# Optimization experiments

Hardware: AMD Instinct MI355X
Metric: run time of the kernel (lower is better)

Reference implementation:

```python
import jax, jax.numpy as jnp
import numpy as np

N_NODES = 50000
N_EDGES = 400000
D = 256
EDGE_DIM = 64
N_LAYERS = 3


def setup_inputs() -> dict:
    key = jax.random.key(0)
    ks = jax.random.split(key, 8)
    sc = 1.0 / np.sqrt(D)
    x = jax.random.normal(ks[0], (N_NODES, D), dtype=jnp.float32)
    edge_attr = jax.random.normal(ks[1], (N_EDGES, EDGE_DIM), dtype=jnp.float32)
    edge_index = jax.random.randint(ks[2], (2, N_EDGES), 0, N_NODES, dtype=jnp.int64)
    Wl = jax.random.normal(ks[3], (N_LAYERS, D, D), dtype=jnp.float32) * sc
    bl = jax.random.normal(ks[4], (N_LAYERS, D), dtype=jnp.float32) * 0.01
    Wr = jax.random.normal(ks[5], (N_LAYERS, D, D), dtype=jnp.float32) * sc
    We = jax.random.normal(ks[6], (N_LAYERS, D, EDGE_DIM), dtype=jnp.float32) * (1.0 / np.sqrt(EDGE_DIM))
    be = jax.random.normal(ks[7], (N_LAYERS, D), dtype=jnp.float32) * 0.01
    return {"x": x, "edge_attr": edge_attr, "edge_index": edge_index,
            "Wl": Wl, "bl": bl, "Wr": Wr, "We": We, "be": be}


def reference(x, edge_attr, edge_index, Wl, bl, Wr, We, be):
    # SAGEConv (mean aggr, root_weight=True, no normalize) with edge-feature
    # augmented messages: msg = x[src] + edge_lin(edge_attr)
    src, dst = edge_index[0], edge_index[1]
    n = x.shape[0]
    # per-target in-degree for mean aggregation (computed once; edge_index fixed)
    deg = jax.ops.segment_sum(jnp.ones((edge_index.shape[1],), x.dtype), dst,
                              num_segments=n)
    inv_deg = (1.0 / jnp.maximum(deg, 1.0))[:, None]  # [N,1]
    for l in range(Wl.shape[0]):
        e_msg = edge_attr @ We[l].T + be[l]                 # [E,D] edge_lin
        msg = x[src] + e_msg                                 # gather + add
        agg = jax.ops.segment_sum(msg, dst, num_segments=n) * inv_deg  # mean
        x = jax.nn.relu(agg @ Wl[l].T + bl[l] + x @ Wr[l].T)
    return x
```

## Files before the change

kernel.cpp:

```cpp
#include <hip/hip_runtime.h>

typedef __attribute__((ext_vector_type(8))) short bf16x8;
typedef __attribute__((ext_vector_type(4))) float f32x4;
typedef unsigned short u16;

#define AS1 __attribute__((address_space(1)))
#define AS3 __attribute__((address_space(3)))

__device__ __forceinline__ u16 f2bf(float f) {
    union { float f; unsigned u; } v; v.f = f;
    unsigned u = v.u;
    return (u16)((u + 0x7FFFu + ((u >> 16) & 1u)) >> 16);
}
__device__ __forceinline__ float bf2f(u16 h) {
    union { unsigned u; float f; } v; v.u = ((unsigned)h) << 16;
    return v.f;
}

__global__ __launch_bounds__(256) void k_convert(const float* __restrict__ x,
                                                 u16* __restrict__ hb, int total4) {
    int i = blockIdx.x * 256 + threadIdx.x;
    if (i >= total4) return;
    float4 v = ((const float4*)x)[i];
    ushort4 o;
    o.x = f2bf(v.x); o.y = f2bf(v.y); o.z = f2bf(v.z); o.w = f2bf(v.w);
    ((ushort4*)hb)[i] = o;
}

__global__ __launch_bounds__(256) void k_count(const int* __restrict__ dst,
                                               int* __restrict__ deg, int E) {
    int e = blockIdx.x * 256 + threadIdx.x;
    if (e < E) atomicAdd(&deg[dst[e]], 1);
}

__global__ __launch_bounds__(256) void k_part(const int* __restrict__ deg,
                                              int* __restrict__ part, int N) {
    __shared__ int ws[4];
    int i = blockIdx.x * 256 + threadIdx.x;
    int v = (i < N) ? deg[i] : 0;
#pragma unroll
    for (int o = 32; o; o >>= 1) v += __shfl_down(v, o);
    int lane = threadIdx.x & 63, w = threadIdx.x >> 6;
    if (lane == 0) ws[w] = v;
    __syncthreads();
    if (threadIdx.x == 0) part[blockIdx.x] = ws[0] + ws[1] + ws[2] + ws[3];
}

__global__ __launch_bounds__(256) void k_scanp(const int* __restrict__ part,
                                               int* __restrict__ bases, int P) {
    __shared__ int s[256];
    int t = threadIdx.x;
    int v = (t < P) ? part[t] : 0;
    s[t] = v;
    __syncthreads();
#pragma unroll
    for (int o = 1; o < 256; o <<= 1) {
        int u = (t >= o) ? s[t - o] : 0;
        __syncthreads();
        s[t] += u;
        __syncthreads();
    }
    bases[t] = s[t] - v;
}

__global__ __launch_bounds__(256) void k_apply(const int* __restrict__ deg,
                                               const int* __restrict__ bases,
                                               int* __restrict__ rp, int* __restrict__ cur,
                                               int N, int E) {
    __shared__ int s[256];
    int b = blockIdx.x, t = threadIdx.x;
    int i = b * 256 + t;
    int d = (i < N) ? deg[i] : 0;
    s[t] = d;
    __syncthreads();
#pragma unroll
    for (int o = 1; o < 256; o <<= 1) {
        int u = (t >= o) ? s[t - o] : 0;
        __syncthreads();
        s[t] += u;
        __syncthreads();
    }
    if (i < N) {
        int r = bases[b] + s[t] - d;
        rp[i] = r;
        cur[i] = r;
    }
    if (b == (int)gridDim.x - 1 && t == 255) rp[N] = E;
}

__global__ __launch_bounds__(256) void k_fill(const int* __restrict__ dst, const int* __restrict__ src,
                                              int* __restrict__ cur,
                                              int* __restrict__ eid, int* __restrict__ srcs, int E) {
    int e = blockIdx.x * 256 + threadIdx.x;
    if (e < E) {
        int p = atomicAdd(&cur[dst[e]], 1);
        eid[p] = e;
        srcs[p] = src[e];
    }
}

__global__ __launch_bounds__(256) void k_sa(const float* __restrict__ attr, const int* __restrict__ rp,
                                            const int* __restrict__ eid, u16* __restrict__ Sa,
                                            unsigned char* __restrict__ hasdeg, int N) {
    int v = blockIdx.x * 4 + (threadIdx.x >> 6);
    if (v >= N) return;
    int l = threadIdx.x & 63;
    int g = l >> 4;
    int c = (l & 15) * 4;
    int j0 = rp[v], j1 = rp[v + 1];
    float4 a = {0.f, 0.f, 0.f, 0.f};
    int jc = j1 - 1;
    for (int j = j0; j < j1; j += 8) {
        int i0 = j + g;
        int i1 = j + 4 + g;
        float m0 = (i0 < j1) ? 1.f : 0.f;
        float m1 = (i1 < j1) ? 1.f : 0.f;
        int e0 = eid[i0 < jc ? i0 : jc];
        int e1 = eid[i1 < jc ? i1 : jc];
        float4 x0 = *(const float4*)&attr[(size_t)e0 * 64 + c];
        float4 x1 = *(const float4*)&attr[(size_t)e1 * 64 + c];
        a.x += m0 * x0.x + m1 * x1.x;
        a.y += m0 * x0.y + m1 * x1.y;
        a.z += m0 * x0.z + m1 * x1.z;
        a.w += m0 * x0.w + m1 * x1.w;
    }
    a.x += __shfl_xor(a.x, 16); a.y += __shfl_xor(a.y, 16);
    a.z += __shfl_xor(a.z, 16); a.w += __shfl_xor(a.w, 16);
    a.x += __shfl_xor(a.x, 32); a.y += __shfl_xor(a.y, 32);
    a.z += __shfl_xor(a.z, 32); a.w += __shfl_xor(a.w, 32);
    int dg = j1 - j0;
    float m = 1.f / (float)(dg > 1 ? dg : 1);
    if (l < 16) {
        ushort4 o;
        o.x = f2bf(a.x * m); o.y = f2bf(a.y * m);
        o.z = f2bf(a.z * m); o.w = f2bf(a.w * m);
        *(ushort4*)&Sa[(size_t)v * 64 + c] = o;
        if (l == 0) hasdeg[v] = (dg > 0) ? 1 : 0;
    }
}

__global__ __launch_bounds__(256) void k_sx(const u16* __restrict__ hb, const int* __restrict__ rp,
                                            const int* __restrict__ srcs,
                                            u16* __restrict__ Sx, int N) {
    int v = blockIdx.x * 4 + (threadIdx.x >> 6);
    if (v >= N) return;
    int l = threadIdx.x & 63;
    int h = l >> 5;
    int c = (l & 31) * 8;
    int j0 = rp[v], j1 = rp[v + 1];
    float a[8] = {0.f, 0.f, 0.f, 0.f, 0.f, 0.f, 0.f, 0.f};
    int jc = j1 - 1;
    for (int j = j0; j < j1; j += 8) {
        int i0 = j + h;
        int i1 = j + 2 + h;
        int i2 = j + 4 + h;
        int i3 = j + 6 + h;
        float m0 = (i0 < j1) ? 1.f : 0.f;
        float m1 = (i1 < j1) ? 1.f : 0.f;
        float m2 = (i2 < j1) ? 1.f : 0.f;
        float m3 = (i3 < j1) ? 1.f : 0.f;
        int s0 = srcs[i0 < jc ? i0 : jc];
        int s1 = srcs[i1 < jc ? i1 : jc];
        int s2 = srcs[i2 < jc ? i2 : jc];
        int s3 = srcs[i3 < jc ? i3 : jc];
        bf16x8 u0 = *(const bf16x8*)&hb[(size_t)s0 * 256 + c];
        bf16x8 u1 = *(const bf16x8*)&hb[(size_t)s1 * 256 + c];
        bf16x8 u2 = *(const bf16x8*)&hb[(size_t)s2 * 256 + c];
        bf16x8 u3 = *(const bf16x8*)&hb[(size_t)s3 * 256 + c];
#pragma unroll
        for (int i = 0; i < 8; ++i)
            a[i] += (m0 * bf2f((u16)u0[i]) + m1 * bf2f((u16)u1[i]))
                  + (m2 * bf2f((u16)u2[i]) + m3 * bf2f((u16)u3[i]));
    }
#pragma unroll
    for (int i = 0; i < 8; ++i) a[i] += __shfl_xor(a[i], 32);
    int dg = j1 - j0;
    float m = 1.f / (float)(dg > 1 ? dg : 1);
    if (l < 32) {
        bf16x8 o;
#pragma unroll
        for (int i = 0; i < 8; ++i) o[i] = (short)f2bf(a[i] * m);
        *(bf16x8*)&Sx[(size_t)v * 256 + c] = o;
    }
}

__global__ __launch_bounds__(256) void k_wprep(const float* __restrict__ Wl, const float* __restrict__ Wr,
                                               const float* __restrict__ We, const float* __restrict__ be,
                                               u16* __restrict__ Wlb, u16* __restrict__ Wrb,
                                               u16* __restrict__ Wleb, float* __restrict__ wlbe) {
    int t = blockIdx.x * 256 + threadIdx.x;
    if (t < 3 * 65536) { Wlb[t] = f2bf(Wl[t]); Wrb[t] = f2bf(Wr[t]); }
    if (t < 3 * 16384) {
        int l = t >> 14;
        int r = t & 16383;
        int d = r >> 6, jj = r & 63;
        const float* wl = Wl + ((size_t)l << 16) + (size_t)d * 256;
        const float* we = We + ((size_t)l << 14) + jj;
        float s = 0.f;
        for (int p = 0; p < 256; ++p) s += wl[p] * we[(size_t)p * 64];
        Wleb[t] = f2bf(s);
    }
    if (t < 768) {
        int l = t >> 8, d = t & 255;
        const float* wl = Wl + ((size_t)l << 16) + (size_t)d * 256;
        const float* b = be + l * 256;
        float s = 0.f;
        for (int p = 0; p < 256; ++p) s += wl[p] * b[p];
        wlbe[t] = s;
    }
}

__device__ __forceinline__ void do_seg(const u16* __restrict__ A, const u16* __restrict__ B,
                                       int lda, int K, int r0, int c0, int M,
                                       u16* Alds, u16* Blds,
                                       int lane, int w, int wr, int wc,
                                       int r16, int kq, f32x4 (&acc)[4][4]) {
    const int rloc = lane >> 3;
    const int cE = (lane & 7) * 8;
    for (int k0 = 0; k0 < K; k0 += 64) {
        __syncthreads();
#pragma unroll
        for (int i = 0; i < 4; ++i) {
            int ch = w * 4 + i;
            int ar = r0 + ch * 8 + rloc;
            ar = ar < M ? ar : M - 1;
            __builtin_amdgcn_global_load_lds(
                (const AS1 void*)(A + (size_t)ar * lda + k0 + cE),
                (AS3 void*)(Alds + ch * 512), 16, 0, 0);
            int br = c0 + ch * 8 + rloc;
            __builtin_amdgcn_global_load_lds(
                (const AS1 void*)(B + (size_t)br * K + k0 + cE),
                (AS3 void*)(Blds + ch * 512), 16, 0, 0);
        }
        __syncthreads();
        bf16x8 af[4][2], bfr[4][2];
#pragma unroll
        for (int rf = 0; rf < 4; ++rf) {
            af[rf][0] = *(const bf16x8*)&Alds[(wr * 64 + rf * 16 + r16) * 64 + kq];
            af[rf][1] = *(const bf16x8*)&Alds[(wr * 64 + rf * 16 + r16) * 64 + 32 + kq];
        }
#pragma unroll
        for (int cf = 0; cf < 4; ++cf) {
            bfr[cf][0] = *(const bf16x8*)&Blds[(wc * 64 + cf * 16 + r16) * 64 + kq];
            bfr[cf][1] = *(const bf16x8*)&Blds[(wc * 64 + cf * 16 + r16) * 64 + 32 + kq];
        }
#pragma unroll
        for (int rf = 0; rf < 4; ++rf)
#pragma unroll
            for (int cf = 0; cf < 4; ++cf) {
                acc[rf][cf] = __builtin_amdgcn_mfma_f32_16x16x32_bf16(af[rf][0], bfr[cf][0], acc[rf][cf], 0, 0, 0);
                acc[rf][cf] = __builtin_amdgcn_mfma_f32_16x16x32_bf16(af[rf][1], bfr[cf][1], acc[rf][cf], 0, 0, 0);
            }
    }
}

__global__ __launch_bounds__(256, 4) void k_gemm(
    const u16* __restrict__ Sx, const u16* __restrict__ Hb, const u16* __restrict__ Sa,
    const u16* __restrict__ Wlb, const u16* __restrict__ Wrb, const u16* __restrict__ Wleb,
    const float* __restrict__ bl, const float* __restrict__ wlbe,
    const unsigned char* __restrict__ hasdeg,
    u16* hb_out, float* f_out, int M)
{
    __shared__ __align__(16) u16 Alds[128 * 64];
    __shared__ __align__(16) u16 Blds[128 * 64];
    const int tid = threadIdx.x;
    const int lane = tid & 63;
    const int w = tid >> 6;
    const int wr = w & 1, wc = w >> 1;
    const int r16 = lane & 15;
    const int hi = lane >> 4;
    const int kq = hi * 8;
    const int rb = blockIdx.x >> 1;
    const int cb = blockIdx.x & 1;
    const int r0 = rb * 128;
    const int c0 = cb * 128;

    const f32x4 fzero = {0.f, 0.f, 0.f, 0.f};
    f32x4 acc[4][4];
#pragma unroll
    for (int a = 0; a < 4; ++a)
#pragma unroll
        for (int b = 0; b < 4; ++b) acc[a][b] = fzero;

    do_seg(Sx, Wlb, 256, 256, r0, c0, M, Alds, Blds, lane, w, wr, wc, r16, kq, acc);
    do_seg(Hb, Wrb, 256, 256, r0, c0, M, Alds, Blds, lane, w, wr, wc, r16, kq, acc);
    do_seg(Sa, Wleb, 64, 64, r0, c0, M, Alds, Blds, lane, w, wr, wc, r16, kq, acc);

    float blv[4], wbev[4];
#pragma unroll
    for (int cf = 0; cf < 4; ++cf) {
        int col = c0 + wc * 64 + 16 * cf + r16;
        blv[cf] = bl[col];
        wbev[cf] = wlbe[col];
    }
#pragma unroll
    for (int rf = 0; rf < 4; ++rf)
#pragma unroll
        for (int j = 0; j < 4; ++j) {
            int r = r0 + wr * 64 + 16 * rf + 4 * hi + j;
            if (r < M) {
                float hd = hasdeg[r] ? 1.f : 0.f;
#pragma unroll
                for (int cf = 0; cf < 4; ++cf) {
                    int col = c0 + wc * 64 + 16 * cf + r16;
                    float v = acc[rf][cf][j] + blv[cf] + hd * wbev[cf];
                    v = fmaxf(v, 0.f);
                    if (f_out) f_out[(size_t)r * 256 + col] = v;
                    if (hb_out) hb_out[(size_t)r * 256 + col] = f2bf(v);
                }
            }
        }
}

extern "C" void kernel_launch(void* const* d_in, const int* in_sizes, int n_in,
                              void* d_out, int out_size, void* d_ws, size_t ws_size,
                              hipStream_t stream) {
    const float* x    = (const float*)d_in[0];
    const float* attr = (const float*)d_in[1];
    const int*   ei   = (const int*)d_in[2];
    const float* Wl   = (const float*)d_in[3];
    const float* bl   = (const float*)d_in[4];
    const float* Wr   = (const float*)d_in[5];
    const float* We   = (const float*)d_in[6];
    const float* be   = (const float*)d_in[7];
    float* out = (float*)d_out;

    const int N = in_sizes[0] / 256;
    const int E = in_sizes[1] / 64;
    const int* srcA = ei;
    const int* dstA = ei + E;

    char* p = (char*)d_ws;
    auto carve = [&](size_t bytes) -> char* {
        char* q = p;
        p += (bytes + 255) & ~(size_t)255;
        return q;
    };
    u16* hb0    = (u16*)carve((size_t)N * 256 * 2);
    u16* hb1    = (u16*)carve((size_t)N * 256 * 2);
    u16* SxB    = (u16*)carve((size_t)N * 256 * 2);
    u16* SaB    = (u16*)carve((size_t)N * 64 * 2);
    u16* Wlb    = (u16*)carve((size_t)3 * 65536 * 2);
    u16* Wrb    = (u16*)carve((size_t)3 * 65536 * 2);
    u16* Wleb   = (u16*)carve((size_t)3 * 16384 * 2);
    float* wlbe = (float*)carve((size_t)3 * 256 * 4);
    int* deg    = (int*)carve((size_t)N * 4);
    int* rp     = (int*)carve((size_t)(N + 1) * 4);
    int* cur    = (int*)carve((size_t)N * 4);
    int* eid    = (int*)carve((size_t)E * 4);
    int* srcs   = (int*)carve((size_t)E * 4);
    int* part   = (int*)carve((size_t)256 * 4);
    int* bases  = (int*)carve((size_t)256 * 4);
    unsigned char* hasdeg = (unsigned char*)carve((size_t)N);

    hipMemsetAsync(deg, 0, (size_t)N * 4, stream);

    int t4 = N * 64;
    k_convert<<<(t4 + 255) / 256, 256, 0, stream>>>(x, hb0, t4);
    k_count<<<(E + 255) / 256, 256, 0, stream>>>(dstA, deg, E);
    const int PB = (N + 255) / 256;
    k_part<<<PB, 256, 0, stream>>>(deg, part, N);
    k_scanp<<<1, 256, 0, stream>>>(part, bases, PB);
    k_apply<<<PB, 256, 0, stream>>>(deg, bases, rp, cur, N, E);
    k_fill<<<(E + 255) / 256, 256, 0, stream>>>(dstA, srcA, cur, eid, srcs, E);
    k_sa<<<(N + 3) / 4, 256, 0, stream>>>(attr, rp, eid, SaB, hasdeg, N);
    k_wprep<<<(3 * 65536 + 255) / 256, 256, 0, stream>>>(Wl, Wr, We, be, Wlb, Wrb, Wleb, wlbe);

    const int RB = (N + 127) / 128;
    const int gblocks = RB * 2;
    u16* hcur = hb0;
    u16* hnxt = hb1;
    for (int l = 0; l < 3; ++l) {
        k_sx<<<(N + 3) / 4, 256, 0, stream>>>(hcur, rp, srcs, SxB, N);
        k_gemm<<<gblocks, 256, 0, stream>>>(SxB, hcur, SaB,
            Wlb + l * 65536, Wrb + l * 65536, Wleb + l * 16384,
            bl + l * 256, wlbe + l * 256, hasdeg,
            (l < 2) ? hnxt : (u16*)nullptr, (l == 2) ? out : (float*)nullptr, N);
        u16* t = hcur; hcur = hnxt; hnxt = t;
    }
}
```

Measured before the change: 319.7 us.

## Cover all 256 output columns per GEMM block with 512 threads

```diff
diff --git a/kernel.cpp b/kernel.cpp
--- a/kernel.cpp
+++ b/kernel.cpp
@@ -210,51 +210,7 @@
     }
 }
 
-__device__ __forceinline__ void do_seg(const u16* __restrict__ A, const u16* __restrict__ B,
-                                       int lda, int K, int r0, int c0, int M,
-                                       u16* Alds, u16* Blds,
-                                       int lane, int w, int wr, int wc,
-                                       int r16, int kq, f32x4 (&acc)[4][4]) {
-    const int rloc = lane >> 3;
-    const int cE = (lane & 7) * 8;
-    for (int k0 = 0; k0 < K; k0 += 64) {
-        __syncthreads();
-#pragma unroll
-        for (int i = 0; i < 4; ++i) {
-            int ch = w * 4 + i;
-            int ar = r0 + ch * 8 + rloc;
-            ar = ar < M ? ar : M - 1;
-            __builtin_amdgcn_global_load_lds(
-                (const AS1 void*)(A + (size_t)ar * lda + k0 + cE),
-                (AS3 void*)(Alds + ch * 512), 16, 0, 0);
-            int br = c0 + ch * 8 + rloc;
-            __builtin_amdgcn_global_load_lds(
-                (const AS1 void*)(B + (size_t)br * K + k0 + cE),
-                (AS3 void*)(Blds + ch * 512), 16, 0, 0);
-        }
-        __syncthreads();
-        bf16x8 af[4][2], bfr[4][2];
-#pragma unroll
-        for (int rf = 0; rf < 4; ++rf) {
-            af[rf][0] = *(const bf16x8*)&Alds[(wr * 64 + rf * 16 + r16) * 64 + kq];
-            af[rf][1] = *(const bf16x8*)&Alds[(wr * 64 + rf * 16 + r16) * 64 + 32 + kq];
-        }
-#pragma unroll
-        for (int cf = 0; cf < 4; ++cf) {
-            bfr[cf][0] = *(const bf16x8*)&Blds[(wc * 64 + cf * 16 + r16) * 64 + kq];
-            bfr[cf][1] = *(const bf16x8*)&Blds[(wc * 64 + cf * 16 + r16) * 64 + 32 + kq];
-        }
-#pragma unroll
-        for (int rf = 0; rf < 4; ++rf)
-#pragma unroll
-            for (int cf = 0; cf < 4; ++cf) {
-                acc[rf][cf] = __builtin_amdgcn_mfma_f32_16x16x32_bf16(af[rf][0], bfr[cf][0], acc[rf][cf], 0, 0, 0);
-                acc[rf][cf] = __builtin_amdgcn_mfma_f32_16x16x32_bf16(af[rf][1], bfr[cf][1], acc[rf][cf], 0, 0, 0);
-            }
-    }
-}
-
-__global__ __launch_bounds__(256, 4) void k_gemm(
+__global__ __launch_bounds__(512, 4) void k_gemm(
     const u16* __restrict__ Sx, const u16* __restrict__ Hb, const u16* __restrict__ Sa,
     const u16* __restrict__ Wlb, const u16* __restrict__ Wrb, const u16* __restrict__ Wleb,
     const float* __restrict__ bl, const float* __restrict__ wlbe,
@@ -262,18 +218,18 @@
     u16* hb_out, float* f_out, int M)
 {
     __shared__ __align__(16) u16 Alds[128 * 64];
-    __shared__ __align__(16) u16 Blds[128 * 64];
+    __shared__ __align__(16) u16 Blds[256 * 64];
     const int tid = threadIdx.x;
     const int lane = tid & 63;
     const int w = tid >> 6;
-    const int wr = w & 1, wc = w >> 1;
+    const int wr = w & 1;
+    const int wc = w >> 1;
     const int r16 = lane & 15;
     const int hi = lane >> 4;
     const int kq = hi * 8;
-    const int rb = blockIdx.x >> 1;
-    const int cb = blockIdx.x & 1;
-    const int r0 = rb * 128;
-    const int c0 = cb * 128;
+    const int r0 = blockIdx.x * 128;
+    const int rloc = lane >> 3;
+    const int cE = (lane & 7) * 8;
 
     const f32x4 fzero = {0.f, 0.f, 0.f, 0.f};
     f32x4 acc[4][4];
@@ -282,14 +238,53 @@
 #pragma unroll
         for (int b = 0; b < 4; ++b) acc[a][b] = fzero;
 
-    do_seg(Sx, Wlb, 256, 256, r0, c0, M, Alds, Blds, lane, w, wr, wc, r16, kq, acc);
-    do_seg(Hb, Wrb, 256, 256, r0, c0, M, Alds, Blds, lane, w, wr, wc, r16, kq, acc);
-    do_seg(Sa, Wleb, 64, 64, r0, c0, M, Alds, Blds, lane, w, wr, wc, r16, kq, acc);
+#pragma unroll
+    for (int t = 0; t < 9; ++t) {
+        const u16* Ag = (t < 4) ? Sx : ((t < 8) ? Hb : Sa);
+        const u16* Bg = (t < 4) ? Wlb : ((t < 8) ? Wrb : Wleb);
+        const int lda = (t < 8) ? 256 : 64;
+        const int Kb = (t < 8) ? 256 : 64;
+        const int k0 = (t < 4) ? t * 64 : ((t < 8) ? (t - 4) * 64 : 0);
+        __syncthreads();
+#pragma unroll
+        for (int i = 0; i < 2; ++i) {
+            int rowb = i * 64 + w * 8;
+            int ar = r0 + rowb + rloc;
+            ar = ar < M ? ar : M - 1;
+            __builtin_amdgcn_global_load_lds(
+                (const AS1 void*)(Ag + (size_t)ar * lda + k0 + cE),
+                (AS3 void*)(&Alds[rowb * 64]), 16, 0, 0);
+        }
+#pragma unroll
+        for (int i = 0; i < 4; ++i) {
+            int rowb = i * 64 + w * 8;
+            __builtin_amdgcn_global_load_lds(
+                (const AS1 void*)(Bg + (size_t)(rowb + rloc) * Kb + k0 + cE),
+                (AS3 void*)(&Blds[rowb * 64]), 16, 0, 0);
+        }
+        __syncthreads();
+        bf16x8 af[4][2];
+#pragma unroll
+        for (int rf = 0; rf < 4; ++rf) {
+            af[rf][0] = *(const bf16x8*)&Alds[(wr * 64 + rf * 16 + r16) * 64 + kq];
+            af[rf][1] = *(const bf16x8*)&Alds[(wr * 64 + rf * 16 + r16) * 64 + 32 + kq];
+        }
+#pragma unroll
+        for (int cf = 0; cf < 4; ++cf) {
+            bf16x8 b0 = *(const bf16x8*)&Blds[(wc * 64 + cf * 16 + r16) * 64 + kq];
+            bf16x8 b1 = *(const bf16x8*)&Blds[(wc * 64 + cf * 16 + r16) * 64 + 32 + kq];
+#pragma unroll
+            for (int rf = 0; rf < 4; ++rf) {
+                acc[rf][cf] = __builtin_amdgcn_mfma_f32_16x16x32_bf16(af[rf][0], b0, acc[rf][cf], 0, 0, 0);
+                acc[rf][cf] = __builtin_amdgcn_mfma_f32_16x16x32_bf16(af[rf][1], b1, acc[rf][cf], 0, 0, 0);
+            }
+        }
+    }
 
     float blv[4], wbev[4];
 #pragma unroll
     for (int cf = 0; cf < 4; ++cf) {
-        int col = c0 + wc * 64 + 16 * cf + r16;
+        int col = wc * 64 + 16 * cf + r16;
         blv[cf] = bl[col];
         wbev[cf] = wlbe[col];
     }
@@ -302,7 +297,7 @@
                 float hd = hasdeg[r] ? 1.f : 0.f;
 #pragma unroll
                 for (int cf = 0; cf < 4; ++cf) {
-                    int col = c0 + wc * 64 + 16 * cf + r16;
+                    int col = wc * 64 + 16 * cf + r16;
                     float v = acc[rf][cf][j] + blv[cf] + hd * wbev[cf];
                     v = fmaxf(v, 0.f);
                     if (f_out) f_out[(size_t)r * 256 + col] = v;
@@ -366,13 +361,12 @@
     k_sa<<<(N + 3) / 4, 256, 0, stream>>>(attr, rp, eid, SaB, hasdeg, N);
     k_wprep<<<(3 * 65536 + 255) / 256, 256, 0, stream>>>(Wl, Wr, We, be, Wlb, Wrb, Wleb, wlbe);
 
-    const int RB = (N + 127) / 128;
-    const int gblocks = RB * 2;
+    const int gblocks = (N + 127) / 128;
     u16* hcur = hb0;
     u16* hnxt = hb1;
     for (int l = 0; l < 3; ++l) {
         k_sx<<<(N + 3) / 4, 256, 0, stream>>>(hcur, rp, srcs, SxB, N);
-        k_gemm<<<gblocks, 256, 0, stream>>>(SxB, hcur, SaB,
+        k_gemm<<<gblocks, 512, 0, stream>>>(SxB, hcur, SaB,
             Wlb + l * 65536, Wrb + l * 65536, Wleb + l * 16384,
             bl + l * 256, wlbe + l * 256, hasdeg,
             (l < 2) ? hnxt : (u16*)nullptr, (l == 2) ? out : (float*)nullptr, N);
```

Result: slower. 351.2 us (+9.9%).
